# Performance work log

Hardware: AMD Instinct MI355X
Metric: run time of the kernel (lower is better)

## Reference

```python
import math
import jax, jax.numpy as jnp
import numpy as np

SR = 22050
W_STEP = 256
W = 2048
TAU_MAX = 2048
MIDI_START = 5
MIDI_END = 85
OCT = 12.0


def _lag_constants():
    # midi -> lag (eq. 4): lag = sr / (440 * 2**((m-69)/12))
    midis = np.arange(MIDI_START, MIDI_END)
    f = 440.0 * np.power(2.0, (midis - 69) / OCT)
    c_ms = SR / f
    return c_ms, np.ceil(c_ms).astype(np.int64), np.floor(c_ms).astype(np.int64)


def setup_inputs() -> dict:
    key = jax.random.key(0)
    x = jax.random.normal(key, (16, 88200), dtype=jnp.float32)
    return {"x": x}


def reference(x):
    B, T = x.shape
    F = (T - W) // W_STEP + 1  # number of frames (unfold with stride w_step)
    idx = jnp.arange(F)[:, None] * W_STEP + jnp.arange(W)[None, :]
    frames = x[:, idx].reshape(B * F, W)  # (BF, W)

    # --- difference function d(tau) via FFT autocorrelation -------------
    x_cumsum = jnp.concatenate(
        [jnp.zeros((B * F, 1), frames.dtype), jnp.cumsum(frames * frames, axis=-1)],
        axis=-1,
    )  # (BF, W+1)
    size = W + TAU_MAX
    p2 = (size // 32).bit_length()
    nice = (16, 18, 20, 24, 25, 27, 30, 32)
    size_pad = min(n * 2 ** p2 for n in nice if n * 2 ** p2 >= size)  # 4096 here
    fc = jnp.fft.rfft(frames, size_pad)
    acf = jnp.fft.irfft(fc * jnp.conj(fc), size_pad)[:, :TAU_MAX]
    df = (
        jnp.flip(x_cumsum[:, W - TAU_MAX + 1 : W + 1], axis=-1)  # x_cumsum[W:W-tau:-1]
        + x_cumsum[:, W : W + 1]
        - x_cumsum[:, :TAU_MAX]
        - 2.0 * acf
    )  # (BF, tau_max)

    # --- cumulative mean normalized difference function (eq. 1/2) -------
    ar = jnp.arange(1, TAU_MAX, dtype=df.dtype)
    cmndf = df[:, 1:] * ar / (jnp.cumsum(df[:, 1:], axis=-1) + 1e-8)
    cmndfs = jnp.concatenate([jnp.ones((B * F, 1), df.dtype), cmndf], axis=-1)

    # --- yingram: linear interpolation at midi lags ----------------------
    c_ms, ceil_i, floor_i = _lag_constants()
    c_ms_j = jnp.asarray(c_ms, dtype=df.dtype)
    denom = jnp.asarray((ceil_i - floor_i), dtype=df.dtype)
    frac = (c_ms_j - jnp.asarray(floor_i, dtype=df.dtype)) / denom
    cf = cmndfs[:, floor_i]
    y = (cmndfs[:, ceil_i] - cf) * frac[None, :] + cf  # (BF, M)

    M = MIDI_END - MIDI_START
    return y.reshape(B, F, M).transpose(0, 2, 1)  # (B, M, F)
```

## Files before the change

### kernel.cpp

```cpp
#include <hip/hip_runtime.h>
#include <math.h>

#define W 2048
#define NB 16
#define TLEN 88200
#define NF 337
#define NMIDI 80

typedef __attribute__((ext_vector_type(8))) short short8;
typedef __attribute__((ext_vector_type(4))) float f32x4;

__device__ __forceinline__ int swix(int t) { return t ^ (((t >> 5) & 7) << 2); }

__device__ __forceinline__ int quadrot(int oct, int s) {
    return (s + 5 * (oct >> 1) + 4 * (oct & 1)) & 7;
}
__device__ __forceinline__ int xoff(int S) {
    int s = S & 7;
    int oct = (S + 256) >> 3;
    return (oct << 6) + (quadrot(oct, s) << 3);
}

__device__ __forceinline__ unsigned int f2bf(float x) {
    unsigned u = __float_as_uint(x);
    u += 0x7FFF + ((u >> 16) & 1);
    return u >> 16;
}

__global__ __launch_bounds__(256) void yin_kernel(const float* __restrict__ x,
                                                  float* __restrict__ out) {
    const int f = blockIdx.x, b = blockIdx.y;
    const int tid = threadIdx.x;
    const int lane = tid & 63, wv = tid >> 6;

    __shared__ unsigned short lds_x[18560];
    __shared__ float cum[2049];
    __shared__ float dfc[2048];
    __shared__ float wsum[4];
    __shared__ float wdsum[4];

    const float* xp = x + (size_t)b * TLEN + (size_t)f * 256;

    float v[16];
    {
        const float4* xq = (const float4*)xp;
        float4 q0 = xq[2 * tid];
        float4 q1 = xq[2 * tid + 1];
        float4 q2 = xq[2 * tid + 2];
        float4 q3 = xq[2 * tid + 3];
        if (tid == 255) {
            q2 = make_float4(0.f, 0.f, 0.f, 0.f);
            q3 = make_float4(0.f, 0.f, 0.f, 0.f);
        }
        v[0]=q0.x; v[1]=q0.y; v[2]=q0.z; v[3]=q0.w;
        v[4]=q1.x; v[5]=q1.y; v[6]=q1.z; v[7]=q1.w;
        v[8]=q2.x; v[9]=q2.y; v[10]=q2.z; v[11]=q2.w;
        v[12]=q3.x; v[13]=q3.y; v[14]=q3.z; v[15]=q3.w;
    }

    float pj[8];
    float etot = 0.f;
    #pragma unroll
    for (int j = 0; j < 8; ++j) { etot = fmaf(v[j], v[j], etot); pj[j] = etot; }

    unsigned D[14];
    #pragma unroll
    for (int i = 0; i < 14; ++i) D[i] = f2bf(v[i]) | (f2bf(v[i + 1]) << 16);
    {
        const int oct = tid + 32;
        const int base = oct << 6;
        #pragma unroll
        for (int s = 0; s < 8; ++s) {
            *(uint4*)(lds_x + base + (quadrot(oct, s) << 3)) =
                make_uint4(D[s], D[s + 2], D[s + 4], D[s + 6]);
        }
    }
    {
        int po = tid >> 3, s = tid & 7;
        *(uint4*)(lds_x + (po << 6) + (quadrot(po, s) << 3)) = make_uint4(0, 0, 0, 0);
        if (tid < 16) {
            int oct2 = 288 + (tid >> 3), s2 = tid & 7;
            *(uint4*)(lds_x + (oct2 << 6) + (quadrot(oct2, s2) << 3)) = make_uint4(0, 0, 0, 0);
        }
    }

    float inc = etot;
    #pragma unroll
    for (int d = 1; d < 64; d <<= 1) {
        float t = __shfl_up(inc, d, 64);
        if (lane >= d) inc += t;
    }
    if (lane == 63) wsum[wv] = inc;

    __syncthreads();

    {
        float base = inc - etot;
        if (wv > 0) base += wsum[0];
        if (wv > 1) base += wsum[1];
        if (wv > 2) base += wsum[2];
        f32x4 q0 = {base, base + pj[0], base + pj[1], base + pj[2]};
        f32x4 q1 = {base + pj[3], base + pj[4], base + pj[5], base + pj[6]};
        *(f32x4*)(cum + swix(8 * tid)) = q0;
        *(f32x4*)(cum + swix(8 * tid + 4)) = q1;
        if (tid == 255) cum[2048] = base + pj[7];
    }

    const int L = lane & 15;
    const int q8 = (lane >> 4) << 3;
    const int bA = 2 * wv;
    const int KA4 = 16 - 4 * wv;

    const unsigned short* pA[4];
    const unsigned short* pB[4];
    #pragma unroll
    for (int i = 0; i < 4; ++i) {
        pA[i] = lds_x + xoff(q8 - 16 * L + 32 * i);
        pB[i] = lds_x + xoff(q8 + L + 256 * bA + 32 * i);
    }

    f32x4 accA = {0.f, 0.f, 0.f, 0.f};
    f32x4 accB = {0.f, 0.f, 0.f, 0.f};
    short8 aM2[4], aM1[4], aC[4], bC[4];

    #pragma unroll
    for (int i = 0; i < 4; ++i) { aM2[i] = *(const short8*)pA[i]; bC[i] = *(const short8*)pB[i]; }
    #pragma unroll
    for (int i = 0; i < 4; ++i) accA = __builtin_amdgcn_mfma_f32_16x16x32_bf16(aM2[i], bC[i], accA, 0, 0, 0);
    #pragma unroll
    for (int i = 0; i < 4; ++i) { aM1[i] = *(const short8*)(pA[i] + 1024); bC[i] = *(const short8*)(pB[i] + 1024); }
    #pragma unroll
    for (int i = 0; i < 4; ++i) accA = __builtin_amdgcn_mfma_f32_16x16x32_bf16(aM1[i], bC[i], accA, 0, 0, 0);

    int go = 2048;
    for (int g = 2; g < KA4; ++g) {
        #pragma unroll
        for (int i = 0; i < 4; ++i) { aC[i] = *(const short8*)(pA[i] + go); bC[i] = *(const short8*)(pB[i] + go); }
        #pragma unroll
        for (int i = 0; i < 4; ++i) {
            accA = __builtin_amdgcn_mfma_f32_16x16x32_bf16(aC[i],  bC[i], accA, 0, 0, 0);
            accB = __builtin_amdgcn_mfma_f32_16x16x32_bf16(aM2[i], bC[i], accB, 0, 0, 0);
        }
        #pragma unroll
        for (int i = 0; i < 4; ++i) { aM2[i] = aM1[i]; aM1[i] = aC[i]; }
        go += 1024;
    }

    __syncthreads();

    {
        const float E = cum[2048];
        const int hi64 = (lane >> 4) << 6;
        #pragma unroll
        for (int r = 0; r < 4; ++r) {
            int tau = (bA << 8) + hi64 + (r << 4) + L;
            dfc[swix(tau)] = cum[swix(2048 - tau)] + E - cum[swix(tau)] - 2.0f * accA[r];
        }
        #pragma unroll
        for (int r = 0; r < 4; ++r) {
            int tau = ((bA + 1) << 8) + hi64 + (r << 4) + L;
            dfc[swix(tau)] = cum[swix(2048 - tau)] + E - cum[swix(tau)] - 2.0f * accB[r];
        }
    }

    __syncthreads();

    float dv[8];
    float excl;
    {
        int t0 = (wv << 9) + (lane << 3);
        f32x4 qa = *(const f32x4*)(dfc + swix(t0));
        f32x4 qb = *(const f32x4*)(dfc + swix(t0 + 4));
        dv[0]=qa.x; dv[1]=qa.y; dv[2]=qa.z; dv[3]=qa.w;
        dv[4]=qb.x; dv[5]=qb.y; dv[6]=qb.z; dv[7]=qb.w;
        if (t0 == 0) dv[0] = 0.f;
        float s = dv[0]+dv[1]+dv[2]+dv[3]+dv[4]+dv[5]+dv[6]+dv[7];
        float inc2 = s;
        #pragma unroll
        for (int d = 1; d < 64; d <<= 1) {
            float tsh = __shfl_up(inc2, d, 64);
            if (lane >= d) inc2 += tsh;
        }
        excl = inc2 - s;
        if (lane == 63) wdsum[wv] = inc2;
    }
    __syncthreads();
    {
        int t0 = (wv << 9) + (lane << 3);
        float run = excl;
        if (wv > 0) run += wdsum[0];
        if (wv > 1) run += wdsum[1];
        if (wv > 2) run += wdsum[2];
        f32x4 qo0, qo1;
        #pragma unroll
        for (int j = 0; j < 8; ++j) {
            run += dv[j];
            float y = (float)(t0 + j) * dv[j] / (run + 1e-8f);
            if (t0 + j == 0) y = 1.0f;
            if (j < 4) qo0[j] = y; else qo1[j - 4] = y;
        }
        *(f32x4*)(dfc + swix(t0)) = qo0;
        *(f32x4*)(dfc + swix(t0 + 4)) = qo1;
    }
    __syncthreads();

    if (tid < NMIDI) {
        float c = 22050.0f / (440.0f * exp2f((float)(tid + 5 - 69) * (1.0f / 12.0f)));
        int fl = (int)c;
        float frac = c - (float)fl;
        float cf = dfc[swix(fl)];
        float cc = dfc[swix(fl + 1)];
        out[(size_t)b * (NMIDI * NF) + (size_t)tid * NF + f] = fmaf(cc - cf, frac, cf);
    }
}

extern "C" void kernel_launch(void* const* d_in, const int* in_sizes, int n_in,
                              void* d_out, int out_size, void* d_ws, size_t ws_size,
                              hipStream_t stream) {
    const float* x = (const float*)d_in[0];
    float* out = (float*)d_out;
    dim3 grid(NF, NB);
    yin_kernel<<<grid, 256, 0, stream>>>(x, out);
}
```

Measured before the change: 103.5 us.

## Process two adjacent frames per block, sharing LDS operand fragments across MFMAs

Each block now handles a pair of frames offset by 256 samples, loading 2304 samples once. The A/B fragments read from LDS feed MFMAs for both frames, with extra pad buffers covering the edge segments, and the cumulative-energy, CMNDF scan and interpolation are done for both frames. This halves the grid and is meant to cut redundant global loads, LDS staging and fixed per-block overhead. In exchange it raises LDS use per block (possibly lowering occupancy), adds register pressure, and needs intricate boundary handling for the odd final frame.

```diff
diff --git a/kernel.cpp b/kernel.cpp
--- a/kernel.cpp
+++ b/kernel.cpp
@@ -5,13 +5,13 @@
 #define NB 16
 #define TLEN 88200
 #define NF 337
+#define NFP 169
 #define NMIDI 80
 
 typedef __attribute__((ext_vector_type(8))) short short8;
 typedef __attribute__((ext_vector_type(4))) float f32x4;
 
 __device__ __forceinline__ int swix(int t) { return t ^ (((t >> 5) & 7) << 2); }
-
 __device__ __forceinline__ int quadrot(int oct, int s) {
     return (s + 5 * (oct >> 1) + 4 * (oct & 1)) & 7;
 }
@@ -20,68 +20,139 @@
     int oct = (S + 256) >> 3;
     return (oct << 6) + (quadrot(oct, s) << 3);
 }
-
 __device__ __forceinline__ unsigned int f2bf(float x) {
     unsigned u = __float_as_uint(x);
     u += 0x7FFF + ((u >> 16) & 1);
     return u >> 16;
 }
 
+#define MM(acc, A_, B_) acc = __builtin_amdgcn_mfma_f32_16x16x32_bf16(A_, B_, acc, 0, 0, 0)
+#define MM4(acc, A_) { MM(acc, A_[0], bF[0]); MM(acc, A_[1], bF[1]); MM(acc, A_[2], bF[2]); MM(acc, A_[3], bF[3]); }
+#define MM4S(acc, A_, B3) { MM(acc, A_[0], bF[0]); MM(acc, A_[1], bF[1]); MM(acc, A_[2], bF[2]); MM(acc, A_[3], B3); }
+#define LDA(dst, gk) { dst[0] = *(const short8*)(lds_x + oA[0] + (gk)*1024); \
+                       dst[1] = *(const short8*)(lds_x + oA[1] + (gk)*1024); \
+                       dst[2] = *(const short8*)(lds_x + oA[2] + (gk)*1024); \
+                       dst[3] = *(const short8*)(lds_x + oA[3] + (gk)*1024); }
+#define LDB(gk)      { bF[0] = *(const short8*)(lds_x + oB[0] + (gk)*1024); \
+                       bF[1] = *(const short8*)(lds_x + oB[1] + (gk)*1024); \
+                       bF[2] = *(const short8*)(lds_x + oB[2] + (gk)*1024); \
+                       bF[3] = *(const short8*)(lds_x + oB[3] + (gk)*1024); }
+
 __global__ __launch_bounds__(256) void yin_kernel(const float* __restrict__ x,
                                                   float* __restrict__ out) {
-    const int f = blockIdx.x, b = blockIdx.y;
+    const int p = blockIdx.x, b = blockIdx.y;
     const int tid = threadIdx.x;
     const int lane = tid & 63, wv = tid >> 6;
-
-    __shared__ unsigned short lds_x[18560];
-    __shared__ float cum[2049];
-    __shared__ float dfc[2048];
+    const bool lastp = (p == NFP - 1);
+
+    __shared__ unsigned short lds_x[20480];
+    __shared__ unsigned short padA[512];
+    __shared__ unsigned short padB0[320];
+    __shared__ unsigned short padB1[320];
+    __shared__ float cumE[2305];
+    __shared__ float dfc[4096];
     __shared__ float wsum[4];
-    __shared__ float wdsum[4];
-
-    const float* xp = x + (size_t)b * TLEN + (size_t)f * 256;
+    __shared__ float wdsum[8];
+
+    const float* xp = x + (size_t)b * TLEN + (size_t)p * 512;
+    const float4* xq = (const float4*)xp;
+    const int elim4 = lastp ? 546 : 0x7FFFFFFF;
 
     float v[16];
     {
-        const float4* xq = (const float4*)xp;
-        float4 q0 = xq[2 * tid];
-        float4 q1 = xq[2 * tid + 1];
-        float4 q2 = xq[2 * tid + 2];
-        float4 q3 = xq[2 * tid + 3];
-        if (tid == 255) {
-            q2 = make_float4(0.f, 0.f, 0.f, 0.f);
-            q3 = make_float4(0.f, 0.f, 0.f, 0.f);
-        }
-        v[0]=q0.x; v[1]=q0.y; v[2]=q0.z; v[3]=q0.w;
-        v[4]=q1.x; v[5]=q1.y; v[6]=q1.z; v[7]=q1.w;
-        v[8]=q2.x; v[9]=q2.y; v[10]=q2.z; v[11]=q2.w;
-        v[12]=q3.x; v[13]=q3.y; v[14]=q3.z; v[15]=q3.w;
-    }
-
+        float4 q[4];
+        #pragma unroll
+        for (int qi = 0; qi < 4; ++qi) {
+            int idx = 2 * tid + qi;
+            q[qi] = (idx < elim4) ? xq[idx] : make_float4(0.f, 0.f, 0.f, 0.f);
+        }
+        v[0]=q[0].x; v[1]=q[0].y; v[2]=q[0].z; v[3]=q[0].w;
+        v[4]=q[1].x; v[5]=q[1].y; v[6]=q[1].z; v[7]=q[1].w;
+        v[8]=q[2].x; v[9]=q[2].y; v[10]=q[2].z; v[11]=q[2].w;
+        v[12]=q[3].x; v[13]=q[3].y; v[14]=q[3].z; v[15]=q[3].w;
+    }
     float pj[8];
     float etot = 0.f;
     #pragma unroll
     for (int j = 0; j < 8; ++j) { etot = fmaf(v[j], v[j], etot); pj[j] = etot; }
-
-    unsigned D[14];
-    #pragma unroll
-    for (int i = 0; i < 14; ++i) D[i] = f2bf(v[i]) | (f2bf(v[i + 1]) << 16);
-    {
+    {
+        unsigned D[14];
+        #pragma unroll
+        for (int i = 0; i < 14; ++i) D[i] = f2bf(v[i]) | (f2bf(v[i + 1]) << 16);
         const int oct = tid + 32;
-        const int base = oct << 6;
-        #pragma unroll
-        for (int s = 0; s < 8; ++s) {
-            *(uint4*)(lds_x + base + (quadrot(oct, s) << 3)) =
+        #pragma unroll
+        for (int s = 0; s < 8; ++s)
+            *(uint4*)(lds_x + (oct << 6) + (quadrot(oct, s) << 3)) =
                 make_uint4(D[s], D[s + 2], D[s + 4], D[s + 6]);
-        }
     }
     {
         int po = tid >> 3, s = tid & 7;
         *(uint4*)(lds_x + (po << 6) + (quadrot(po, s) << 3)) = make_uint4(0, 0, 0, 0);
-        if (tid < 16) {
-            int oct2 = 288 + (tid >> 3), s2 = tid & 7;
-            *(uint4*)(lds_x + (oct2 << 6) + (quadrot(oct2, s2) << 3)) = make_uint4(0, 0, 0, 0);
-        }
+    }
+    float p2j[8];
+    if (tid < 32) {
+        float v2[16];
+        float4 q[4];
+        #pragma unroll
+        for (int qi = 0; qi < 4; ++qi) {
+            int idx = 512 + 2 * tid + qi;
+            q[qi] = (idx < elim4) ? xq[idx] : make_float4(0.f, 0.f, 0.f, 0.f);
+        }
+        v2[0]=q[0].x; v2[1]=q[0].y; v2[2]=q[0].z; v2[3]=q[0].w;
+        v2[4]=q[1].x; v2[5]=q[1].y; v2[6]=q[1].z; v2[7]=q[1].w;
+        v2[8]=q[2].x; v2[9]=q[2].y; v2[10]=q[2].z; v2[11]=q[2].w;
+        v2[12]=q[3].x; v2[13]=q[3].y; v2[14]=q[3].z; v2[15]=q[3].w;
+        float e2 = 0.f;
+        #pragma unroll
+        for (int j = 0; j < 8; ++j) { e2 = fmaf(v2[j], v2[j], e2); p2j[j] = e2; }
+        unsigned D2[14];
+        #pragma unroll
+        for (int i = 0; i < 14; ++i) D2[i] = f2bf(v2[i]) | (f2bf(v2[i + 1]) << 16);
+        const int oct = 288 + tid;
+        #pragma unroll
+        for (int s = 0; s < 8; ++s)
+            *(uint4*)(lds_x + (oct << 6) + (quadrot(oct, s) << 3)) =
+                make_uint4(D2[s], D2[s + 2], D2[s + 4], D2[s + 6]);
+    }
+    if (tid >= 64 && tid < 104) {
+        int S = 2016 + (tid - 64);
+        int oc = S >> 3, s = S & 7;
+        unsigned u[8];
+        #pragma unroll
+        for (int j = 0; j < 8; ++j) {
+            int e = S + j;
+            float val = (e < 2048) ? xp[e] : 0.0f;
+            u[j] = f2bf(val);
+        }
+        *(uint4*)(padB0 + ((oc - 252) << 6) + (quadrot(oc, s) << 3)) =
+            make_uint4(u[0]|(u[1]<<16), u[2]|(u[3]<<16), u[4]|(u[5]<<16), u[6]|(u[7]<<16));
+    }
+    if (tid >= 104 && tid < 144) {
+        int S = 2272 + (tid - 104);
+        int oc = S >> 3, s = S & 7;
+        unsigned u[8];
+        #pragma unroll
+        for (int j = 0; j < 8; ++j) {
+            int e = S + j;
+            float val = 0.0f;
+            if (!lastp && e < 2304) val = xp[e];
+            u[j] = f2bf(val);
+        }
+        *(uint4*)(padB1 + ((oc - 284) << 6) + (quadrot(oc, s) << 3)) =
+            make_uint4(u[0]|(u[1]<<16), u[2]|(u[3]<<16), u[4]|(u[5]<<16), u[6]|(u[7]<<16));
+    }
+    if (tid >= 144 && tid < 206) {
+        int w = tid - 144;
+        int t0 = -240 + 8 * w;
+        unsigned u[8];
+        #pragma unroll
+        for (int j = 0; j < 8; ++j) {
+            int t = t0 + j;
+            float val = (t >= 0) ? xp[256 + t] : 0.0f;
+            u[j] = f2bf(val);
+        }
+        *(uint4*)(padA + 8 * w) =
+            make_uint4(u[0]|(u[1]<<16), u[2]|(u[3]<<16), u[4]|(u[5]<<16), u[6]|(u[7]<<16));
     }
 
     float inc = etot;
@@ -101,116 +172,199 @@
         if (wv > 2) base += wsum[2];
         f32x4 q0 = {base, base + pj[0], base + pj[1], base + pj[2]};
         f32x4 q1 = {base + pj[3], base + pj[4], base + pj[5], base + pj[6]};
-        *(f32x4*)(cum + swix(8 * tid)) = q0;
-        *(f32x4*)(cum + swix(8 * tid + 4)) = q1;
-        if (tid == 255) cum[2048] = base + pj[7];
+        *(f32x4*)(cumE + swix(8 * tid)) = q0;
+        *(f32x4*)(cumE + swix(8 * tid + 4)) = q1;
+    }
+    if (tid < 32) {
+        float E2048 = wsum[0] + wsum[1] + wsum[2] + wsum[3];
+        float e2tot = p2j[7];
+        float inc2 = e2tot;
+        #pragma unroll
+        for (int d = 1; d < 32; d <<= 1) {
+            float t = __shfl_up(inc2, d, 64);
+            if (lane >= d) inc2 += t;
+        }
+        float baseE = E2048 + inc2 - e2tot;
+        f32x4 q0 = {baseE, baseE + p2j[0], baseE + p2j[1], baseE + p2j[2]};
+        f32x4 q1 = {baseE + p2j[3], baseE + p2j[4], baseE + p2j[5], baseE + p2j[6]};
+        *(f32x4*)(cumE + swix(2048 + 8 * tid)) = q0;
+        *(f32x4*)(cumE + swix(2048 + 8 * tid + 4)) = q1;
+        if (tid == 31) cumE[2304] = baseE + p2j[7];
     }
 
     const int L = lane & 15;
     const int q8 = (lane >> 4) << 3;
     const int bA = 2 * wv;
     const int KA4 = 16 - 4 * wv;
-
-    const unsigned short* pA[4];
-    const unsigned short* pB[4];
+    const int P = KA4 >> 2;
+    const bool w3 = (wv == 3);
+
+    int oA[4], oB[4];
     #pragma unroll
     for (int i = 0; i < 4; ++i) {
-        pA[i] = lds_x + xoff(q8 - 16 * L + 32 * i);
-        pB[i] = lds_x + xoff(q8 + L + 256 * bA + 32 * i);
-    }
-
-    f32x4 accA = {0.f, 0.f, 0.f, 0.f};
-    f32x4 accB = {0.f, 0.f, 0.f, 0.f};
-    short8 aM2[4], aM1[4], aC[4], bC[4];
-
+        oA[i] = xoff(32 * i + q8 - 16 * L);
+        oB[i] = xoff(32 * i + q8 + L + 256 * bA);
+    }
+    const int SB0 = 2016 + q8 + L;
+    const int oPB0 = (((SB0 >> 3) - 252) << 6) + (quadrot(SB0 >> 3, SB0 & 7) << 3);
+    const int SB1 = 2272 + q8 + L;
+    const int oPB1 = (((SB1 >> 3) - 284) << 6) + (quadrot(SB1 >> 3, SB1 & 7) << 3);
+
+    short8 sA0[4], sA1[4], sA2[4], sA3[4], aP2[4], aP3[4], bF[4];
     #pragma unroll
-    for (int i = 0; i < 4; ++i) { aM2[i] = *(const short8*)pA[i]; bC[i] = *(const short8*)pB[i]; }
-    #pragma unroll
-    for (int i = 0; i < 4; ++i) accA = __builtin_amdgcn_mfma_f32_16x16x32_bf16(aM2[i], bC[i], accA, 0, 0, 0);
-    #pragma unroll
-    for (int i = 0; i < 4; ++i) { aM1[i] = *(const short8*)(pA[i] + 1024); bC[i] = *(const short8*)(pB[i] + 1024); }
-    #pragma unroll
-    for (int i = 0; i < 4; ++i) accA = __builtin_amdgcn_mfma_f32_16x16x32_bf16(aM1[i], bC[i], accA, 0, 0, 0);
-
-    int go = 2048;
-    for (int g = 2; g < KA4; ++g) {
-        #pragma unroll
-        for (int i = 0; i < 4; ++i) { aC[i] = *(const short8*)(pA[i] + go); bC[i] = *(const short8*)(pB[i] + go); }
-        #pragma unroll
-        for (int i = 0; i < 4; ++i) {
-            accA = __builtin_amdgcn_mfma_f32_16x16x32_bf16(aC[i],  bC[i], accA, 0, 0, 0);
-            accB = __builtin_amdgcn_mfma_f32_16x16x32_bf16(aM2[i], bC[i], accB, 0, 0, 0);
-        }
-        #pragma unroll
-        for (int i = 0; i < 4; ++i) { aM2[i] = aM1[i]; aM1[i] = aC[i]; }
-        go += 1024;
-    }
-
-    __syncthreads();
-
-    {
-        const float E = cum[2048];
+    for (int i = 0; i < 4; ++i) {
+        aP2[i] = *(const short8*)(padA + (256 + 32 * i + q8 - 16 * L) - 16);
+        aP3[i] = *(const short8*)(padA + (384 + 32 * i + q8 - 16 * L) - 16);
+    }
+    short8 bp0 = *(const short8*)(padB0 + oPB0);
+
+    f32x4 acc0A = {0.f,0.f,0.f,0.f}, acc0B = {0.f,0.f,0.f,0.f};
+    f32x4 acc1A = {0.f,0.f,0.f,0.f}, acc1B = {0.f,0.f,0.f,0.f};
+
+    LDA(sA0, 0); LDB(0); MM4(acc0A, sA0);
+    LDA(sA1, 1); LDB(1); MM4(acc0A, sA1);
+    LDA(sA2, 2); LDB(2);
+    MM4(acc0A, sA2); MM4(acc0B, sA0); MM4(acc1A, aP2);
+    LDA(sA3, 3); LDB(3);
+    {
+        short8 b3 = w3 ? bp0 : bF[3];
+        MM4S(acc0A, sA3, b3); MM4S(acc0B, sA1, b3); MM4(acc1A, aP3);
+    }
+    LDA(sA0, 4); LDB(4);
+    if (!w3) { MM4(acc0A, sA0); MM4(acc0B, sA2); }
+    MM4(acc1A, sA0); MM4(acc1B, aP2);
+    LDA(sA1, 5);
+    {
+        bF[0] = *(const short8*)(lds_x + oB[0] + 5 * 1024);
+        bF[1] = *(const short8*)(lds_x + oB[1] + 5 * 1024);
+        bF[2] = *(const short8*)(lds_x + oB[2] + 5 * 1024);
+        const unsigned short* pb3 = w3 ? (padB1 + oPB1) : (lds_x + oB[3] + 5 * 1024);
+        bF[3] = *(const short8*)pb3;
+    }
+    if (!w3) { MM4(acc0A, sA1); MM4(acc0B, sA3); }
+    MM4(acc1A, sA1); MM4(acc1B, aP3);
+
+    for (int pp = 1; pp < P; ++pp) {
+        const int g0 = 2 + 4 * pp;
+        const bool lastP = (pp == P - 1);
+        LDA(sA2, g0); LDB(g0);
+        MM4(acc0A, sA2); MM4(acc0B, sA0); MM4(acc1A, sA2); MM4(acc1B, sA0);
+        LDA(sA3, g0 + 1); LDB(g0 + 1);
+        {
+            short8 b3 = lastP ? bp0 : bF[3];
+            MM4S(acc0A, sA3, b3); MM4S(acc0B, sA1, b3);
+            MM4(acc1A, sA3); MM4(acc1B, sA1);
+        }
+        LDA(sA0, g0 + 2); LDB(g0 + 2);
+        if (!lastP) { MM4(acc0A, sA0); MM4(acc0B, sA2); }
+        MM4(acc1A, sA0); MM4(acc1B, sA2);
+        LDA(sA1, g0 + 3);
+        {
+            bF[0] = *(const short8*)(lds_x + oB[0] + (g0 + 3) * 1024);
+            bF[1] = *(const short8*)(lds_x + oB[1] + (g0 + 3) * 1024);
+            bF[2] = *(const short8*)(lds_x + oB[2] + (g0 + 3) * 1024);
+            const unsigned short* pb3 = lastP ? (padB1 + oPB1)
+                                              : (lds_x + oB[3] + (g0 + 3) * 1024);
+            bF[3] = *(const short8*)pb3;
+        }
+        if (!lastP) { MM4(acc0A, sA1); MM4(acc0B, sA3); }
+        MM4(acc1A, sA1); MM4(acc1B, sA3);
+    }
+
+    __syncthreads();
+
+    {
         const int hi64 = (lane >> 4) << 6;
-        #pragma unroll
-        for (int r = 0; r < 4; ++r) {
-            int tau = (bA << 8) + hi64 + (r << 4) + L;
-            dfc[swix(tau)] = cum[swix(2048 - tau)] + E - cum[swix(tau)] - 2.0f * accA[r];
-        }
-        #pragma unroll
-        for (int r = 0; r < 4; ++r) {
-            int tau = ((bA + 1) << 8) + hi64 + (r << 4) + L;
-            dfc[swix(tau)] = cum[swix(2048 - tau)] + E - cum[swix(tau)] - 2.0f * accB[r];
-        }
-    }
-
-    __syncthreads();
-
-    float dv[8];
-    float excl;
+        {
+            const float cW = cumE[2048], c0 = cumE[0];
+            #pragma unroll
+            for (int r = 0; r < 4; ++r) {
+                int tau = (bA << 8) + hi64 + (r << 4) + L;
+                dfc[swix(tau)] = cumE[swix(2048 - tau)] + cW - cumE[swix(tau)] - c0 - 2.0f * acc0A[r];
+            }
+            #pragma unroll
+            for (int r = 0; r < 4; ++r) {
+                int tau = ((bA + 1) << 8) + hi64 + (r << 4) + L;
+                dfc[swix(tau)] = cumE[swix(2048 - tau)] + cW - cumE[swix(tau)] - c0 - 2.0f * acc0B[r];
+            }
+        }
+        {
+            const float cW = cumE[2304], c0 = cumE[swix(256)];
+            #pragma unroll
+            for (int r = 0; r < 4; ++r) {
+                int tau = (bA << 8) + hi64 + (r << 4) + L;
+                dfc[2048 + swix(tau)] = cumE[swix(2304 - tau)] + cW - cumE[swix(tau + 256)] - c0 - 2.0f * acc1A[r];
+            }
+            #pragma unroll
+            for (int r = 0; r < 4; ++r) {
+                int tau = ((bA + 1) << 8) + hi64 + (r << 4) + L;
+                dfc[2048 + swix(tau)] = cumE[swix(2304 - tau)] + cW - cumE[swix(tau + 256)] - c0 - 2.0f * acc1B[r];
+            }
+        }
+    }
+
+    __syncthreads();
+
+    float dv0[8], dv1[8], ex0, ex1;
     {
         int t0 = (wv << 9) + (lane << 3);
         f32x4 qa = *(const f32x4*)(dfc + swix(t0));
         f32x4 qb = *(const f32x4*)(dfc + swix(t0 + 4));
-        dv[0]=qa.x; dv[1]=qa.y; dv[2]=qa.z; dv[3]=qa.w;
-        dv[4]=qb.x; dv[5]=qb.y; dv[6]=qb.z; dv[7]=qb.w;
-        if (t0 == 0) dv[0] = 0.f;
-        float s = dv[0]+dv[1]+dv[2]+dv[3]+dv[4]+dv[5]+dv[6]+dv[7];
-        float inc2 = s;
+        f32x4 qc = *(const f32x4*)(dfc + 2048 + swix(t0));
+        f32x4 qd = *(const f32x4*)(dfc + 2048 + swix(t0 + 4));
+        dv0[0]=qa.x; dv0[1]=qa.y; dv0[2]=qa.z; dv0[3]=qa.w;
+        dv0[4]=qb.x; dv0[5]=qb.y; dv0[6]=qb.z; dv0[7]=qb.w;
+        dv1[0]=qc.x; dv1[1]=qc.y; dv1[2]=qc.z; dv1[3]=qc.w;
+        dv1[4]=qd.x; dv1[5]=qd.y; dv1[6]=qd.z; dv1[7]=qd.w;
+        if (t0 == 0) { dv0[0] = 0.f; dv1[0] = 0.f; }
+        float s0 = dv0[0]+dv0[1]+dv0[2]+dv0[3]+dv0[4]+dv0[5]+dv0[6]+dv0[7];
+        float s1 = dv1[0]+dv1[1]+dv1[2]+dv1[3]+dv1[4]+dv1[5]+dv1[6]+dv1[7];
+        float i0 = s0, i1 = s1;
         #pragma unroll
         for (int d = 1; d < 64; d <<= 1) {
-            float tsh = __shfl_up(inc2, d, 64);
-            if (lane >= d) inc2 += tsh;
-        }
-        excl = inc2 - s;
-        if (lane == 63) wdsum[wv] = inc2;
+            float t0s = __shfl_up(i0, d, 64);
+            float t1s = __shfl_up(i1, d, 64);
+            if (lane >= d) { i0 += t0s; i1 += t1s; }
+        }
+        ex0 = i0 - s0; ex1 = i1 - s1;
+        if (lane == 63) { wdsum[wv] = i0; wdsum[4 + wv] = i1; }
     }
     __syncthreads();
     {
         int t0 = (wv << 9) + (lane << 3);
-        float run = excl;
-        if (wv > 0) run += wdsum[0];
-        if (wv > 1) run += wdsum[1];
-        if (wv > 2) run += wdsum[2];
-        f32x4 qo0, qo1;
+        float run0 = ex0, run1 = ex1;
+        if (wv > 0) { run0 += wdsum[0]; run1 += wdsum[4]; }
+        if (wv > 1) { run0 += wdsum[1]; run1 += wdsum[5]; }
+        if (wv > 2) { run0 += wdsum[2]; run1 += wdsum[6]; }
+        f32x4 o0a, o0b, o1a, o1b;
         #pragma unroll
         for (int j = 0; j < 8; ++j) {
-            run += dv[j];
-            float y = (float)(t0 + j) * dv[j] / (run + 1e-8f);
-            if (t0 + j == 0) y = 1.0f;
-            if (j < 4) qo0[j] = y; else qo1[j - 4] = y;
-        }
-        *(f32x4*)(dfc + swix(t0)) = qo0;
-        *(f32x4*)(dfc + swix(t0 + 4)) = qo1;
-    }
-    __syncthreads();
-
-    if (tid < NMIDI) {
-        float c = 22050.0f / (440.0f * exp2f((float)(tid + 5 - 69) * (1.0f / 12.0f)));
-        int fl = (int)c;
-        float frac = c - (float)fl;
-        float cf = dfc[swix(fl)];
-        float cc = dfc[swix(fl + 1)];
-        out[(size_t)b * (NMIDI * NF) + (size_t)tid * NF + f] = fmaf(cc - cf, frac, cf);
+            run0 += dv0[j];
+            run1 += dv1[j];
+            float y0 = (float)(t0 + j) * dv0[j] / (run0 + 1e-8f);
+            float y1 = (float)(t0 + j) * dv1[j] / (run1 + 1e-8f);
+            if (t0 + j == 0) { y0 = 1.0f; y1 = 1.0f; }
+            if (j < 4) { o0a[j] = y0; o1a[j] = y1; } else { o0b[j-4] = y0; o1b[j-4] = y1; }
+        }
+        *(f32x4*)(dfc + swix(t0)) = o0a;
+        *(f32x4*)(dfc + swix(t0 + 4)) = o0b;
+        *(f32x4*)(dfc + 2048 + swix(t0)) = o1a;
+        *(f32x4*)(dfc + 2048 + swix(t0 + 4)) = o1b;
+    }
+    __syncthreads();
+
+    if (tid < 2 * NMIDI) {
+        int j = (tid >= NMIDI) ? 1 : 0;
+        int m = tid - NMIDI * j;
+        int fr = 2 * p + j;
+        if (fr < NF) {
+            float c = 22050.0f / (440.0f * exp2f((float)(m - 64) * (1.0f / 12.0f)));
+            int fl = (int)c;
+            float frac = c - (float)fl;
+            float cf = dfc[(j << 11) + swix(fl)];
+            float cc = dfc[(j << 11) + swix(fl + 1)];
+            out[(size_t)b * (NMIDI * NF) + (size_t)m * NF + fr] = fmaf(cc - cf, frac, cf);
+        }
     }
 }
 
@@ -219,6 +373,6 @@
                               hipStream_t stream) {
     const float* x = (const float*)d_in[0];
     float* out = (float*)d_out;
-    dim3 grid(NF, NB);
+    dim3 grid(NFP, NB);
     yin_kernel<<<grid, 256, 0, stream>>>(x, out);
 }
```

Measured after the change: 104.4 us. About the same (+1.0%).
